# Performance work log

Measured on AMD Instinct MI355X. Metric: run time of the kernel, lower is better.

The kernel has to match this reference:

```python
import jax, jax.numpy as jnp
import numpy as np

B, S, HID = 2, 2048, 2048
H, KVH, D = 16, 8, 128           # query heads, kv heads, head_dim
G = H // KVH                      # num_key_value_groups
EPS = 1e-6
SCALE = D ** -0.5
ROPE_THETA = 1e6


def _rope_tables():
    inv_freq = 1.0 / (ROPE_THETA ** (jnp.arange(0, D, 2, dtype=jnp.float32) / D))
    freqs = jnp.arange(S, dtype=jnp.float32)[:, None] * inv_freq[None, :]   # [S, D/2]
    emb = jnp.concatenate([freqs, freqs], axis=-1)                          # [S, D]
    cos = jnp.broadcast_to(jnp.cos(emb)[None], (B, S, D))
    sin = jnp.broadcast_to(jnp.sin(emb)[None], (B, S, D))
    return cos, sin


def setup_inputs() -> dict:
    key = jax.random.key(0)
    ks = jax.random.split(key, 6)
    hidden_states = jax.random.normal(ks[0], (B, S, HID), jnp.float32)
    cos, sin = _rope_tables()
    w = 0.02
    Wq = jax.random.normal(ks[1], (HID, H * D * 2), jnp.float32) * w  # gated: q + gate
    Wk = jax.random.normal(ks[2], (HID, KVH * D), jnp.float32) * w
    Wv = jax.random.normal(ks[3], (HID, KVH * D), jnp.float32) * w
    Wo = jax.random.normal(ks[4], (H * D, HID), jnp.float32) * w
    q_norm_w = jnp.ones((D,), jnp.float32)
    k_norm_w = jnp.ones((D,), jnp.float32)
    return {"hidden_states": hidden_states, "cos": cos, "sin": sin,
            "Wq": Wq, "Wk": Wk, "Wv": Wv, "Wo": Wo,
            "q_norm_w": q_norm_w, "k_norm_w": k_norm_w}


def _rms_norm(x, w):
    # per-head RMSNorm over last dim (head_dim), computed in fp32
    var = jnp.mean(jnp.square(x.astype(jnp.float32)), axis=-1, keepdims=True)
    return (x * jax.lax.rsqrt(var + EPS)) * w


def _rotate_half(x):
    x1, x2 = x[..., : D // 2], x[..., D // 2:]
    return jnp.concatenate([-x2, x1], axis=-1)


def reference(hidden_states, cos, sin, Wq, Wk, Wv, Wo, q_norm_w, k_norm_w):
    # q_proj with output gate
    mixed_q = hidden_states @ Wq                         # [B,S,H*2D]
    mixed_q = mixed_q.reshape(B, S, H, 2 * D)
    q, gate = mixed_q[..., :D], mixed_q[..., D:]          # [B,S,H,D] each
    gate = gate.reshape(B, S, H * D)
    k = (hidden_states @ Wk).reshape(B, S, KVH, D)
    v = (hidden_states @ Wv).reshape(B, S, KVH, D)

    # per-head QK RMSNorm, then to [B, heads, S, D]
    q = _rms_norm(q, q_norm_w).transpose(0, 2, 1, 3)      # [B,H,S,D]
    k = _rms_norm(k, k_norm_w).transpose(0, 2, 1, 3)      # [B,KVH,S,D]
    v = v.transpose(0, 2, 1, 3)                           # [B,KVH,S,D]

    # RoPE (cos/sin broadcast over head dim)
    c, s = cos[:, None], sin[:, None]                     # [B,1,S,D]
    q = q * c + _rotate_half(q) * s
    k = k * c + _rotate_half(k) * s

    # GQA causal attention without materializing repeated K/V
    qg = q.reshape(B, KVH, G, S, D)
    scores = jnp.einsum('bkgqd,bkld->bkgql', qg, k) * SCALE   # [B,KVH,G,S,S]
    causal = jnp.tril(jnp.ones((S, S), dtype=bool))
    scores = jnp.where(causal, scores, jnp.finfo(scores.dtype).min)
    probs = jax.nn.softmax(scores, axis=-1)
    out = jnp.einsum('bkgql,bkld->bkgqd', probs, v)           # [B,KVH,G,S,D]
    out = out.reshape(B, H, S, D).transpose(0, 2, 1, 3).reshape(B, S, H * D)

    # sigmoid-gated output, then o_proj
    out = out * jax.nn.sigmoid(gate)
    return out @ Wo
```

## Files before the change

### kernel.cpp

```cpp
#include <hip/hip_runtime.h>
#include <hip/hip_bf16.h>

#define B_ 2
#define S_ 2048
#define HID_ 2048
#define H_ 16
#define KVH_ 8
#define D_ 128
#define G_ 2
#define EPS_ 1e-6f
#define SCALE_ 0.08838834764831845f
#define SCALE2_ 0.1275313760443445f
#define NQKV 6144

typedef __hip_bfloat16 bf16;
typedef __attribute__((ext_vector_type(8))) short s8v;
typedef __attribute__((ext_vector_type(4))) float f4v;

__device__ __forceinline__ unsigned short f2b(float f) {
    __hip_bfloat16 h = __float2bfloat16(f);
    return *reinterpret_cast<unsigned short*>(&h);
}
__device__ __forceinline__ float b2f(short u) {
    unsigned int x = ((unsigned int)(unsigned short)u) << 16;
    return __builtin_bit_cast(float, x);
}

__device__ __forceinline__ f4v MFMA(s8v a, s8v b, f4v c) {
    return __builtin_amdgcn_mfma_f32_16x16x32_bf16(a, b, c, 0, 0, 0);
}

__device__ __forceinline__ void gl_lds16(const void* g, void* l) {
    __builtin_amdgcn_global_load_lds(
        (const __attribute__((address_space(1))) void*)g,
        (__attribute__((address_space(3))) void*)l, 16, 0, 0);
}

__device__ __forceinline__ void cstore(float* p, float v) { *p = v; }
__device__ __forceinline__ void cstore(short* p, float v) { *p = (short)f2b(v); }

template <int CTRL>
__device__ __forceinline__ float dpp_f(float x) {
    return __builtin_bit_cast(float,
        __builtin_amdgcn_update_dpp(0, __builtin_bit_cast(int, x), CTRL, 0xF, 0xF, true));
}
__device__ __forceinline__ float red16_max(float v) {
    v = fmaxf(v, dpp_f<0xB1>(v));
    v = fmaxf(v, dpp_f<0x4E>(v));
    v = fmaxf(v, dpp_f<0x124>(v));
    v = fmaxf(v, dpp_f<0x128>(v));
    return v;
}
__device__ __forceinline__ float red16_sum(float v) {
    v += dpp_f<0xB1>(v);
    v += dpp_f<0x4E>(v);
    v += dpp_f<0x124>(v);
    v += dpp_f<0x128>(v);
    return v;
}

__global__ __launch_bounds__(256) void f2bf_kernel(const float* __restrict__ in,
                                                   short* __restrict__ out, int n4) {
    int i = blockIdx.x * 256 + threadIdx.x;
    if (i >= n4) return;
    const float4 v = *(const float4*)(in + (size_t)i * 4);
    ushort4 o;
    o.x = f2b(v.x); o.y = f2b(v.y); o.z = f2b(v.z); o.w = f2b(v.w);
    *(ushort4*)(out + (size_t)i * 4) = o;
}

__global__ __launch_bounds__(256) void transpose_conv(const float* __restrict__ in,
                                                      short* __restrict__ out,
                                                      int K, int N) {
    __shared__ short t[32][33];
    const int n0 = blockIdx.x * 32, k0 = blockIdx.y * 32;
    const int tx = threadIdx.x, ty = threadIdx.y;
#pragma unroll
    for (int j = 0; j < 4; j++) {
        const int r = ty + j * 8;
        t[r][tx] = (short)f2b(in[(size_t)(k0 + r) * N + n0 + tx]);
    }
    __syncthreads();
#pragma unroll
    for (int j = 0; j < 4; j++) {
        const int r = ty + j * 8;
        out[(size_t)(n0 + r) * K + k0 + tx] = t[tx][r];
    }
}

__global__ __launch_bounds__(256) void transpose_v(const short* __restrict__ in,
                                                   short* __restrict__ out) {
    __shared__ short t[32][33];
    const int s0 = blockIdx.x * 32, d0 = blockIdx.y * 32, bk = blockIdx.z;
    const int b = bk / KVH_, kvh = bk % KVH_;
    const short* ip = in + (size_t)b * S_ * NQKV + kvh * D_;
    const int tx = threadIdx.x, ty = threadIdx.y;
#pragma unroll
    for (int j = 0; j < 4; j++) {
        const int r = ty + j * 8;
        t[r][tx] = ip[(size_t)(s0 + r) * NQKV + d0 + tx];
    }
    __syncthreads();
#pragma unroll
    for (int j = 0; j < 4; j++) {
        const int r = ty + j * 8;
        out[((size_t)bk * D_ + d0 + r) * S_ + s0 + tx] = t[tx][r];
    }
}

template <typename CT, int GATED>
__global__ __launch_bounds__(256) void gemm_bt(const short* __restrict__ A,
                                               const short* __restrict__ Bt,
                                               CT* __restrict__ C,
                                               int M, int N, int K) {
    __shared__ __align__(16) short As[2][128][32];
    __shared__ __align__(16) short Bs[2][128][32];
    const int tid = threadIdx.x;
    const int w = tid >> 6, l = tid & 63;
    const int lr = l & 15, g = l >> 4;
    const int nwg = gridDim.x * gridDim.y;
    int bid = blockIdx.y * gridDim.x + blockIdx.x;
    bid = (bid & 7) * (nwg >> 3) + (bid >> 3);
    const int bx = bid % gridDim.x, by = bid / gridDim.x;
    const int row0 = by * 128, col0 = bx * 128;
    const int wr = w >> 1, wc = w & 1;

    f4v acc[4][4];
#pragma unroll
    for (int i = 0; i < 4; i++)
#pragma unroll
        for (int j = 0; j < 4; j++) acc[i][j] = (f4v)0.f;

    const int srow = l >> 2;
    const int sg = (l & 3) ^ ((srow >> 1) & 3);

    auto stage = [&](int buf, int kt) {
        const int k = kt + sg * 8;
#pragma unroll
        for (int i = 0; i < 2; i++) {
            const int rb = (w * 2 + i) * 16;
            size_t aoff;
            if constexpr (GATED)
                aoff = (size_t)(row0 + rb + srow) * NQKV + ((k >> 7) << 8) + (k & 127);
            else
                aoff = (size_t)(row0 + rb + srow) * K + k;
            gl_lds16(A + aoff, &As[buf][rb][0]);
            gl_lds16(Bt + (size_t)(col0 + rb + srow) * K + k, &Bs[buf][rb][0]);
        }
    };

    const int nt = K >> 5;
    stage(0, 0);
    stage(1, 32);
    const int rdslot = (g ^ ((lr >> 1) & 3)) * 8;

#pragma unroll 1
    for (int t = 0; t < nt; t++) {
        const int cur = t & 1;
        if (t + 1 < nt) {
            asm volatile("s_waitcnt vmcnt(4)" ::: "memory");
        } else {
            asm volatile("s_waitcnt vmcnt(0)" ::: "memory");
        }
        __builtin_amdgcn_s_barrier();
        __builtin_amdgcn_sched_barrier(0);

        s8v a[4], b[4];
#pragma unroll
        for (int mi = 0; mi < 4; mi++)
            a[mi] = *(const s8v*)&As[cur][wr * 64 + mi * 16 + lr][rdslot];
#pragma unroll
        for (int ni = 0; ni < 4; ni++)
            b[ni] = *(const s8v*)&Bs[cur][wc * 64 + ni * 16 + lr][rdslot];

        asm volatile("s_waitcnt lgkmcnt(0)" ::: "memory");
        __builtin_amdgcn_sched_barrier(0);
        __builtin_amdgcn_s_barrier();
        __builtin_amdgcn_sched_barrier(0);

        if (t + 2 < nt) stage(cur, (t + 2) * 32);

#pragma unroll
        for (int mi = 0; mi < 4; mi++)
#pragma unroll
            for (int ni = 0; ni < 4; ni++)
                acc[mi][ni] = MFMA(a[mi], b[ni], acc[mi][ni]);
    }

#pragma unroll
    for (int mi = 0; mi < 4; mi++)
#pragma unroll
        for (int ni = 0; ni < 4; ni++) {
            const int row = row0 + wr * 64 + mi * 16 + g * 4;
            const int col = col0 + wc * 64 + ni * 16 + lr;
#pragma unroll
            for (int j = 0; j < 4; j++)
                cstore(&C[(size_t)(row + j) * N + col], acc[mi][ni][j]);
        }
}

__global__ __launch_bounds__(128) void norm_rope(const bf16* __restrict__ src,
                                                 const float* __restrict__ normw,
                                                 const float* __restrict__ cosb,
                                                 const float* __restrict__ sinb,
                                                 bf16* __restrict__ dst,
                                                 int NH, int rowStride, int chanStride) {
    const int idx = blockIdx.x;
    const int h = idx % NH;
    const int s = (idx / NH) % S_;
    const int b = idx / (NH * S_);
    const int d = threadIdx.x;

    const size_t src_i = (size_t)(b * S_ + s) * rowStride + h * chanStride + d;
    const size_t dst_i = (((size_t)b * NH + h) * S_ + s) * D_ + d;

    float x = __bfloat162float(src[src_i]);
    float sq = x * x;
#pragma unroll
    for (int o = 32; o > 0; o >>= 1) sq += __shfl_down(sq, o);
    __shared__ float red[2];
    __shared__ float sh[128];
    if ((d & 63) == 0) red[d >> 6] = sq;
    __syncthreads();
    const float var = (red[0] + red[1]) * (1.f / 128.f);
    const float xn = x * rsqrtf(var + EPS_) * normw[d];
    sh[d] = xn;
    __syncthreads();
    const float rot = (d < 64) ? -sh[d + 64] : sh[d - 64];
    const size_t cs_i = ((size_t)b * S_ + s) * D_ + d;
    dst[dst_i] = __float2bfloat16(xn * cosb[cs_i] + rot * sinb[cs_i]);
}

__global__ __launch_bounds__(256) void flash_mfma(const short* __restrict__ qro,
                                                  const short* __restrict__ kro,
                                                  const short* __restrict__ vt,
                                                  short* __restrict__ qkv) {
    __shared__ __align__(16) short Ks[2][64][128];
    __shared__ __align__(16) short Vs[2][128][64];
    __shared__ __align__(16) short Pl[4][16][84];

    const int tid = threadIdx.x;
    const int w = tid >> 6, l = tid & 63;
    const int lr = l & 15, g = l >> 4;
    const int bx = blockIdx.x;
    const int bh = blockIdx.y;
    const int b = bh >> 4, h = bh & 15;
    const int kvh = h >> 1;

    const short* qbase = qro + (size_t)(b * H_ + h) * S_ * D_;
    const short* kbase = kro + (size_t)(b * KVH_ + kvh) * S_ * D_;
    const short* vbase = vt + (size_t)(b * KVH_ + kvh) * D_ * S_;

    auto stage = [&](int buf, int kt) {
        const int kb0 = kt * 64;
#pragma unroll
        for (int i = 0; i < 4; i++) {
            const int li = w * 4 + i;
            {
                const int r = li * 4 + (l >> 4);
                const int sgk = (l & 15) ^ (r & 7);
                gl_lds16(kbase + (size_t)(kb0 + r) * D_ + sgk * 8, &Ks[buf][li * 4][0]);
            }
            {
                const int r = li * 8 + (l >> 3);
                const int sgv = (l & 7) ^ (r & 7);
                gl_lds16(vbase + (size_t)r * S_ + kb0 + sgv * 8, &Vs[buf][li * 8][0]);
            }
        }
    };

#pragma unroll 1
    for (int seg = 0; seg < 2; seg++) {
        const int qt = seg ? bx : (31 - bx);
        const int q0 = qt * 64;
        const int qw0 = q0 + w * 16;

        if (seg) __syncthreads();

        s8v qa[4];
#pragma unroll
        for (int kc = 0; kc < 4; kc++)
            qa[kc] = *(const s8v*)(qbase + (size_t)(qw0 + lr) * D_ + kc * 32 + g * 8);

        f4v oacc[8];
#pragma unroll
        for (int i = 0; i < 8; i++) oacc[i] = (f4v)0.f;
        float m[4] = {-3e38f, -3e38f, -3e38f, -3e38f};
        float lsum[4] = {0.f, 0.f, 0.f, 0.f};

        const int nkt = qt + 1;
        stage(0, 0);
        int cur = 0;
        for (int kt = 0; kt < nkt; kt++) {
            __syncthreads();
            if (kt + 1 < nkt) stage(cur ^ 1, kt + 1);
            const int kb0 = kt * 64;

            f4v sacc[4];
#pragma unroll
            for (int ni = 0; ni < 4; ni++) sacc[ni] = (f4v)0.f;
            __builtin_amdgcn_s_setprio(1);
#pragma unroll
            for (int ni = 0; ni < 4; ni++) {
                const int r = ni * 16 + lr;
#pragma unroll
                for (int kc = 0; kc < 4; kc++) {
                    const int ph = (kc * 4 + g) ^ (r & 7);
                    const s8v kb = *(const s8v*)&Ks[cur][r][ph * 8];
                    sacc[ni] = MFMA(qa[kc], kb, sacc[ni]);
                }
            }
            __builtin_amdgcn_s_setprio(0);

            const bool masked = (kt == qt);
            float p[4][4], tmax[4];
#pragma unroll
            for (int j = 0; j < 4; j++) {
                float v0 = -3e38f;
#pragma unroll
                for (int ni = 0; ni < 4; ni++) {
                    float sc = sacc[ni][j] * SCALE2_;
                    if (masked && (kb0 + ni * 16 + lr > qw0 + g * 4 + j)) sc = -3e38f;
                    p[ni][j] = sc;
                    v0 = fmaxf(v0, sc);
                }
                tmax[j] = v0;
            }
#pragma unroll
            for (int j = 0; j < 4; j++) tmax[j] = red16_max(tmax[j]);

            bool needb = false;
#pragma unroll
            for (int j = 0; j < 4; j++) needb = needb || (tmax[j] > m[j] + 7.f);
            const bool doresc = __any((int)needb);

            float cj[4], psum[4];
#pragma unroll
            for (int j = 0; j < 4; j++) {
                float mn = m[j];
                if (doresc) {
                    mn = fmaxf(m[j], tmax[j]);
                    cj[j] = __builtin_amdgcn_exp2f(m[j] - mn);
                    m[j] = mn;
                }
                float ps = 0.f;
#pragma unroll
                for (int ni = 0; ni < 4; ni++) {
                    const float e = __builtin_amdgcn_exp2f(p[ni][j] - mn);
                    p[ni][j] = e;
                    ps += e;
                }
                psum[j] = ps;
            }

#pragma unroll
            for (int ni = 0; ni < 4; ni++)
#pragma unroll
                for (int j = 0; j < 4; j++)
                    Pl[w][g * 4 + j][ni * 16 + lr] = (short)f2b(p[ni][j]);

#pragma unroll
            for (int j = 0; j < 4; j++) psum[j] = red16_sum(psum[j]);

            if (doresc) {
#pragma unroll
                for (int j = 0; j < 4; j++) lsum[j] = lsum[j] * cj[j] + psum[j];
#pragma unroll
                for (int di = 0; di < 8; di++)
#pragma unroll
                    for (int j = 0; j < 4; j++) oacc[di][j] *= cj[j];
            } else {
#pragma unroll
                for (int j = 0; j < 4; j++) lsum[j] += psum[j];
            }

            __builtin_amdgcn_s_setprio(1);
#pragma unroll
            for (int kk = 0; kk < 2; kk++) {
                const s8v pa = *(const s8v*)&Pl[w][lr][kk * 32 + g * 8];
#pragma unroll
                for (int di = 0; di < 8; di++) {
                    const int r = di * 16 + lr;
                    const int ph = (kk * 4 + g) ^ (r & 7);
                    const s8v vb = *(const s8v*)&Vs[cur][r][ph * 8];
                    oacc[di] = MFMA(pa, vb, oacc[di]);
                }
            }
            __builtin_amdgcn_s_setprio(0);
            cur ^= 1;
        }

        float linv[4];
#pragma unroll
        for (int j = 0; j < 4; j++) linv[j] = 1.f / lsum[j];
#pragma unroll
        for (int di = 0; di < 8; di++) {
            const int d = di * 16 + lr;
#pragma unroll
            for (int j = 0; j < 4; j++) {
                const int q = qw0 + g * 4 + j;
                const size_t base = (size_t)(b * S_ + q) * NQKV + h * 256;
                const float gate = b2f(qkv[base + 128 + d]);
                const float o = oacc[di][j] * linv[j] * (1.f / (1.f + __expf(-gate)));
                qkv[base + d] = (short)f2b(o);
            }
        }
    }
}

extern "C" void kernel_launch(void* const* d_in, const int* in_sizes, int n_in,
                              void* d_out, int out_size, void* d_ws, size_t ws_size,
                              hipStream_t stream) {
    const float* hs = (const float*)d_in[0];
    const float* cosb = (const float*)d_in[1];
    const float* sinb = (const float*)d_in[2];
    const float* Wq = (const float*)d_in[3];
    const float* Wk = (const float*)d_in[4];
    const float* Wv = (const float*)d_in[5];
    const float* Wo = (const float*)d_in[6];
    const float* qnw = (const float*)d_in[7];
    const float* knw = (const float*)d_in[8];
    float* out = (float*)d_out;

    short* ws = (short*)d_ws;
    short* Wot = ws;
    short* Wt  = ws + 4194304;
    short* hsb = ws + 16777216;
    short* qkv = ws + 25165824;
    short* qro = Wt;
    short* kro = Wt + 8388608;
    short* vtb = hsb;

    const int M = B_ * S_;
    const dim3 t32x8(32, 8, 1);

    f2bf_kernel<<<8192, 256, 0, stream>>>(hs, hsb, 2097152);
    transpose_conv<<<dim3(128, 64), t32x8, 0, stream>>>(Wq, Wt, HID_, 4096);
    transpose_conv<<<dim3(32, 64), t32x8, 0, stream>>>(Wk, Wt + (size_t)4096 * 2048, HID_, 1024);
    transpose_conv<<<dim3(32, 64), t32x8, 0, stream>>>(Wv, Wt + (size_t)5120 * 2048, HID_, 1024);
    transpose_conv<<<dim3(64, 64), t32x8, 0, stream>>>(Wo, Wot, 2048, 2048);

    gemm_bt<short, 0><<<dim3(48, 32), 256, 0, stream>>>(hsb, Wt, qkv, M, NQKV, HID_);

    norm_rope<<<dim3(B_ * S_ * H_), 128, 0, stream>>>((const bf16*)qkv, qnw, cosb, sinb,
                                                      (bf16*)qro, H_, NQKV, 256);
    norm_rope<<<dim3(B_ * S_ * KVH_), 128, 0, stream>>>((const bf16*)(qkv + 4096), knw, cosb, sinb,
                                                        (bf16*)kro, KVH_, NQKV, 128);

    transpose_v<<<dim3(64, 4, 16), t32x8, 0, stream>>>(qkv + 5120, vtb);

    flash_mfma<<<dim3(16, 32), 256, 0, stream>>>(qro, kro, vtb, qkv);

    gemm_bt<float, 1><<<dim3(16, 32), 256, 0, stream>>>(qkv, Wot, out, M, HID_, 2048);
}
```

Before: 328.0 us.

## Use 256x256-tile triple-buffered GEMM for fused QKV projection

Adds a new bf16 MFMA GEMM kernel with 256x256 output tiles, 512 threads (8 waves, each computing 128x64), and a three-stage LDS ring buffer. Global-to-LDS loads for the A and B tiles are interleaved between two half-steps of MFMAs, with s_setprio used to raise priority around the MFMA blocks. The fused QKV projection switches to this kernel. The aim is more data reuse per tile and better overlap of loads with compute, at the cost of higher register and LDS use and only 384 workgroups, which may underfill the GPU's compute units.

```diff
diff --git a/kernel.cpp b/kernel.cpp
--- a/kernel.cpp
+++ b/kernel.cpp
@@ -106,6 +106,114 @@
         const int r = ty + j * 8;
         out[((size_t)bk * D_ + d0 + r) * S_ + s0 + tx] = t[tx][r];
     }
+}
+
+__global__ __launch_bounds__(512, 2) void gemm256(const short* __restrict__ A,
+                                                  const short* __restrict__ Bt,
+                                                  short* __restrict__ C,
+                                                  int M, int N, int K) {
+    __shared__ __align__(16) short As[3][256][32];
+    __shared__ __align__(16) short Bs[3][256][32];
+    const int tid = threadIdx.x;
+    const int w = tid >> 6, l = tid & 63;
+    const int lr = l & 15, g = l >> 4;
+    const int nwg = gridDim.x * gridDim.y;
+    int bid = blockIdx.y * gridDim.x + blockIdx.x;
+    bid = (bid & 7) * (nwg >> 3) + (bid >> 3);
+    const int bx = bid % gridDim.x, by = bid / gridDim.x;
+    const int row0 = by * 256, col0 = bx * 256;
+    const int wr = w >> 2, wc = w & 3;
+
+    f4v acc[8][4];
+#pragma unroll
+    for (int i = 0; i < 8; i++)
+#pragma unroll
+        for (int j = 0; j < 4; j++) acc[i][j] = (f4v)0.f;
+
+    const int srow = l >> 2;
+    const int schunk = (l & 3) ^ ((l >> 3) & 3);
+    const int rdslot = (g ^ ((lr >> 1) & 3)) * 8;
+
+    auto stageA = [&](int buf, int t) {
+        const int kt = t * 32;
+#pragma unroll
+        for (int i = 0; i < 2; i++) {
+            const int rb = w * 32 + i * 16;
+            gl_lds16(A + (size_t)(row0 + rb + srow) * K + kt + schunk * 8,
+                     &As[buf][rb][0]);
+        }
+    };
+    auto stageB = [&](int buf, int t) {
+        const int kt = t * 32;
+#pragma unroll
+        for (int i = 0; i < 2; i++) {
+            const int rb = w * 32 + i * 16;
+            gl_lds16(Bt + (size_t)(col0 + rb + srow) * K + kt + schunk * 8,
+                     &Bs[buf][rb][0]);
+        }
+    };
+
+    const int nt = K >> 5;
+    stageA(0, 0); stageB(0, 0);
+    stageA(1, 1); stageB(1, 1);
+
+#pragma unroll 1
+    for (int t = 0; t < nt; t++) {
+        const int buf = t % 3;
+        const int nbuf = (t + 2) % 3;
+
+        __builtin_amdgcn_sched_barrier(0);
+        if (t + 1 < nt) {
+            asm volatile("s_waitcnt vmcnt(4)" ::: "memory");
+        } else {
+            asm volatile("s_waitcnt vmcnt(0)" ::: "memory");
+        }
+        __builtin_amdgcn_sched_barrier(0);
+        __builtin_amdgcn_s_barrier();
+        __builtin_amdgcn_sched_barrier(0);
+
+        s8v b[4], a[4];
+#pragma unroll
+        for (int ni = 0; ni < 4; ni++)
+            b[ni] = *(const s8v*)&Bs[buf][wc * 64 + ni * 16 + lr][rdslot];
+#pragma unroll
+        for (int mi = 0; mi < 4; mi++)
+            a[mi] = *(const s8v*)&As[buf][wr * 128 + mi * 16 + lr][rdslot];
+        if (t + 2 < nt) stageA(nbuf, t + 2);
+        __builtin_amdgcn_s_setprio(1);
+#pragma unroll
+        for (int mi = 0; mi < 4; mi++)
+#pragma unroll
+            for (int ni = 0; ni < 4; ni++)
+                acc[mi][ni] = MFMA(a[mi], b[ni], acc[mi][ni]);
+        __builtin_amdgcn_s_setprio(0);
+        __builtin_amdgcn_s_barrier();
+        __builtin_amdgcn_sched_barrier(0);
+
+        s8v a2[4];
+#pragma unroll
+        for (int mi = 0; mi < 4; mi++)
+            a2[mi] = *(const s8v*)&As[buf][wr * 128 + (4 + mi) * 16 + lr][rdslot];
+        if (t + 2 < nt) stageB(nbuf, t + 2);
+        __builtin_amdgcn_s_setprio(1);
+#pragma unroll
+        for (int mi = 0; mi < 4; mi++)
+#pragma unroll
+            for (int ni = 0; ni < 4; ni++)
+                acc[4 + mi][ni] = MFMA(a2[mi], b[ni], acc[4 + mi][ni]);
+        __builtin_amdgcn_s_setprio(0);
+    }
+
+#pragma unroll
+    for (int mi = 0; mi < 8; mi++)
+#pragma unroll
+        for (int ni = 0; ni < 4; ni++) {
+            const int row = row0 + wr * 128 + mi * 16 + g * 4;
+            const int col = col0 + wc * 64 + ni * 16 + lr;
+#pragma unroll
+            for (int j = 0; j < 4; j++)
+                cstore(&C[(size_t)(row + j) * N + col], acc[mi][ni][j]);
+        }
 }
 
 template <typename CT, int GATED>
@@ -440,7 +548,7 @@
     transpose_conv<<<dim3(32, 64), t32x8, 0, stream>>>(Wv, Wt + (size_t)5120 * 2048, HID_, 1024);
     transpose_conv<<<dim3(64, 64), t32x8, 0, stream>>>(Wo, Wot, 2048, 2048);
 
-    gemm_bt<short, 0><<<dim3(48, 32), 256, 0, stream>>>(hsb, Wt, qkv, M, NQKV, HID_);
+    gemm256<<<dim3(24, 16), 512, 0, stream>>>(hsb, Wt, qkv, M, NQKV, HID_);
 
     norm_rope<<<dim3(B_ * S_ * H_), 128, 0, stream>>>((const bf16*)qkv, qnw, cosb, sinb,
                                                       (bf16*)qro, H_, NQKV, 256);
```

After: 326.0 us. Within noise of the previous version (-0.6%).

## Rework projection GEMMs into 256x128 tiles with 4-stage pipeline and fragment prefetch

Applied to the files above, without the earlier changes.

The projection GEMM kernel now uses 512-thread blocks computing 256x128 output tiles. It keeps a 4-slot LDS ring with three stages in flight and double-buffers register fragments so LDS reads for the next step overlap the current MFMAs, raising wave priority during MFMA. The goal is to hide global load latency, cut barrier stalls and improve B-tile reuse. In exchange it doubles LDS per block, and for the output projection it halves the block count to 256, which risks under-filling the GPU.

```diff
diff --git a/kernel.cpp b/kernel.cpp
--- a/kernel.cpp
+++ b/kernel.cpp
@@ -109,12 +109,12 @@
 }
 
 template <typename CT, int GATED>
-__global__ __launch_bounds__(256) void gemm_bt(const short* __restrict__ A,
-                                               const short* __restrict__ Bt,
-                                               CT* __restrict__ C,
-                                               int M, int N, int K) {
-    __shared__ __align__(16) short As[2][128][32];
-    __shared__ __align__(16) short Bs[2][128][32];
+__global__ __launch_bounds__(512, 2) void gemm_dp(const short* __restrict__ A,
+                                                  const short* __restrict__ Bt,
+                                                  CT* __restrict__ C,
+                                                  int M, int N, int K) {
+    __shared__ __align__(16) short As[4][256][32];
+    __shared__ __align__(16) short Bs[4][128][32];
     const int tid = threadIdx.x;
     const int w = tid >> 6, l = tid & 63;
     const int lr = l & 15, g = l >> 4;
@@ -122,7 +122,7 @@
     int bid = blockIdx.y * gridDim.x + blockIdx.x;
     bid = (bid & 7) * (nwg >> 3) + (bid >> 3);
     const int bx = bid % gridDim.x, by = bid / gridDim.x;
-    const int row0 = by * 128, col0 = bx * 128;
+    const int row0 = by * 256, col0 = bx * 128;
     const int wr = w >> 1, wc = w & 1;
 
     f4v acc[4][4];
@@ -131,60 +131,77 @@
 #pragma unroll
         for (int j = 0; j < 4; j++) acc[i][j] = (f4v)0.f;
 
+    const int rdslot = (g ^ ((lr >> 1) & 3)) * 8;
     const int srow = l >> 2;
-    const int sg = (l & 3) ^ ((srow >> 1) & 3);
-
-    auto stage = [&](int buf, int kt) {
-        const int k = kt + sg * 8;
-#pragma unroll
-        for (int i = 0; i < 2; i++) {
-            const int rb = (w * 2 + i) * 16;
+    const int schunk = (l & 3) ^ ((l >> 3) & 3);
+
+    const int SP = K >> 5;
+
+    auto stage = [&](int s) {
+        const int slot = s & 3;
+        const int kb = s * 32 + schunk * 8;
+#pragma unroll
+        for (int j = 0; j < 2; j++) {
+            const int r = (j * 8 + w) * 16;
+            const int grow = row0 + r + srow;
             size_t aoff;
             if constexpr (GATED)
-                aoff = (size_t)(row0 + rb + srow) * NQKV + ((k >> 7) << 8) + (k & 127);
+                aoff = (size_t)grow * NQKV + ((kb >> 7) << 8) + (kb & 127);
             else
-                aoff = (size_t)(row0 + rb + srow) * K + k;
-            gl_lds16(A + aoff, &As[buf][rb][0]);
-            gl_lds16(Bt + (size_t)(col0 + rb + srow) * K + k, &Bs[buf][rb][0]);
-        }
+                aoff = (size_t)grow * K + kb;
+            gl_lds16(A + aoff, &As[slot][r][0]);
+        }
+        gl_lds16(Bt + (size_t)(col0 + w * 16 + srow) * K + kb, &Bs[slot][w * 16][0]);
     };
 
-    const int nt = K >> 5;
-    stage(0, 0);
-    stage(1, 32);
-    const int rdslot = (g ^ ((lr >> 1) & 3)) * 8;
-
-#pragma unroll 1
-    for (int t = 0; t < nt; t++) {
-        const int cur = t & 1;
-        if (t + 1 < nt) {
-            asm volatile("s_waitcnt vmcnt(4)" ::: "memory");
+    auto frags = [&](int s, s8v* a, s8v* b) {
+        const int slot = s & 3;
+#pragma unroll
+        for (int mi = 0; mi < 4; mi++)
+            a[mi] = *(const s8v*)&As[slot][wr * 64 + mi * 16 + lr][rdslot];
+#pragma unroll
+        for (int ni = 0; ni < 4; ni++)
+            b[ni] = *(const s8v*)&Bs[slot][wc * 64 + ni * 16 + lr][rdslot];
+    };
+
+    stage(0); stage(1); stage(2);
+    __builtin_amdgcn_sched_barrier(0);
+    asm volatile("s_waitcnt vmcnt(6)" ::: "memory");
+    __builtin_amdgcn_sched_barrier(0);
+    __builtin_amdgcn_s_barrier();
+    __builtin_amdgcn_sched_barrier(0);
+
+    s8v aA[4], bA[4], aB[4], bB[4];
+    frags(0, aA, bA);
+
+    auto phase = [&](int s, s8v* au, s8v* bu, s8v* an, s8v* bn) {
+        __builtin_amdgcn_sched_barrier(0);
+        if (s + 3 <= SP) {
+            asm volatile("s_waitcnt vmcnt(3)" ::: "memory");
         } else {
             asm volatile("s_waitcnt vmcnt(0)" ::: "memory");
         }
-        __builtin_amdgcn_s_barrier();
-        __builtin_amdgcn_sched_barrier(0);
-
-        s8v a[4], b[4];
-#pragma unroll
-        for (int mi = 0; mi < 4; mi++)
-            a[mi] = *(const s8v*)&As[cur][wr * 64 + mi * 16 + lr][rdslot];
-#pragma unroll
-        for (int ni = 0; ni < 4; ni++)
-            b[ni] = *(const s8v*)&Bs[cur][wc * 64 + ni * 16 + lr][rdslot];
-
-        asm volatile("s_waitcnt lgkmcnt(0)" ::: "memory");
         __builtin_amdgcn_sched_barrier(0);
         __builtin_amdgcn_s_barrier();
         __builtin_amdgcn_sched_barrier(0);
-
-        if (t + 2 < nt) stage(cur, (t + 2) * 32);
-
+        asm volatile("s_waitcnt lgkmcnt(0)" ::: "memory");
+        __builtin_amdgcn_sched_barrier(0);
+        if (s + 3 < SP) stage(s + 3);
+        __builtin_amdgcn_s_setprio(1);
 #pragma unroll
         for (int mi = 0; mi < 4; mi++)
 #pragma unroll
             for (int ni = 0; ni < 4; ni++)
-                acc[mi][ni] = MFMA(a[mi], b[ni], acc[mi][ni]);
+                acc[mi][ni] = MFMA(au[mi], bu[ni], acc[mi][ni]);
+        __builtin_amdgcn_s_setprio(0);
+        __builtin_amdgcn_sched_barrier(0);
+        if (s + 1 < SP) frags(s + 1, an, bn);
+    };
+
+#pragma unroll 1
+    for (int s = 0; s < SP; s += 2) {
+        phase(s, aA, bA, aB, bB);
+        phase(s + 1, aB, bB, aA, bA);
     }
 
 #pragma unroll
@@ -440,7 +457,7 @@
     transpose_conv<<<dim3(32, 64), t32x8, 0, stream>>>(Wv, Wt + (size_t)5120 * 2048, HID_, 1024);
     transpose_conv<<<dim3(64, 64), t32x8, 0, stream>>>(Wo, Wot, 2048, 2048);
 
-    gemm_bt<short, 0><<<dim3(48, 32), 256, 0, stream>>>(hsb, Wt, qkv, M, NQKV, HID_);
+    gemm_dp<short, 0><<<dim3(48, 16), 512, 0, stream>>>(hsb, Wt, qkv, M, NQKV, HID_);
 
     norm_rope<<<dim3(B_ * S_ * H_), 128, 0, stream>>>((const bf16*)qkv, qnw, cosb, sinb,
                                                       (bf16*)qro, H_, NQKV, 256);
@@ -451,5 +468,5 @@
 
     flash_mfma<<<dim3(16, 32), 256, 0, stream>>>(qro, kro, vtb, qkv);
 
-    gemm_bt<float, 1><<<dim3(16, 32), 256, 0, stream>>>(qkv, Wot, out, M, HID_, 2048);
-}
+    gemm_dp<float, 1><<<dim3(16, 16), 512, 0, stream>>>(qkv, Wot, out, M, HID_, 2048);
+}
```

Result: slower. 357.5 us (+9.0%).
